# Performance work log

Hardware: AMD Instinct MI355X
Metric: run time of the kernel (lower is better)

The kernel has to match this reference:

```python
import math
import jax, jax.numpy as jnp
import numpy as np

B, C, H, W = 64, 1536, 16, 16
M_CLUSTERS, L_DIM, G_DIM, HID = 64, 128, 256, 512


def setup_inputs() -> dict:
    key = jax.random.key(0)
    ks = jax.random.split(key, 10)

    def w(k, out_d, in_d):
        return jax.random.normal(k, (out_d, in_d), jnp.float32) * (1.0 / np.sqrt(in_d))

    return {
        "x": jax.random.normal(ks[0], (B, C, H, W), jnp.float32),
        "t": jax.random.normal(ks[1], (B, C), jnp.float32),
        # token_features: Linear(C,512) -> ReLU -> Linear(512, token_dim)
        "Wt1": w(ks[2], HID, C), "bt1": jnp.zeros((HID,), jnp.float32),
        "Wt2": w(ks[3], G_DIM, HID), "bt2": jnp.zeros((G_DIM,), jnp.float32),
        # cluster_features: Conv1x1(C,512) -> ReLU -> Conv1x1(512, cluster_dim)
        "Wc1": w(ks[4], HID, C), "bc1": jnp.zeros((HID,), jnp.float32),
        "Wc2": w(ks[5], L_DIM, HID), "bc2": jnp.zeros((L_DIM,), jnp.float32),
        # score: Conv1x1(C,512) -> ReLU -> Conv1x1(512, num_clusters)
        "Ws1": w(ks[6], HID, C), "bs1": jnp.zeros((HID,), jnp.float32),
        "Ws2": w(ks[7], M_CLUSTERS, HID), "bs2": jnp.zeros((M_CLUSTERS,), jnp.float32),
        "dust_bin": jnp.float32(1.0),
    }


def _l2norm(a, axis):
    n = jnp.maximum(jnp.linalg.norm(a, axis=axis, keepdims=True), 1e-12)
    return a / n


def _conv1x1_mlp(xf, W1, b1, W2, b2):
    # xf: [B, C, N]; 1x1 convs are channel GEMMs
    h = jax.nn.relu(jnp.einsum('oc,bcn->bon', W1, xf) + b1[None, :, None])
    return jnp.einsum('oc,bcn->bon', W2, h) + b2[None, :, None]


def _matching_probs(S, dust_bin, num_iters=3):
    # Sinkhorn with dustbin row (log domain), reg = 1.0
    b, m, n = S.shape
    dust_row = jnp.broadcast_to(dust_bin.astype(S.dtype), (b, 1, n))
    Ms = jnp.concatenate([S, dust_row], axis=1)  # [B, m+1, n]
    norm = -math.log(n + m)
    log_a = jnp.full((m + 1,), norm, S.dtype).at[-1].add(math.log(n - m))
    log_b = jnp.full((n,), norm, S.dtype)
    u = jnp.zeros((b, m + 1), S.dtype)
    v = jnp.zeros((b, n), S.dtype)
    for _ in range(num_iters):
        u = log_a[None, :] - jax.scipy.special.logsumexp(Ms + v[:, None, :], axis=2)
        v = log_b[None, :] - jax.scipy.special.logsumexp(Ms + u[:, :, None], axis=1)
    return Ms + u[:, :, None] + v[:, None, :] - norm  # log_P - norm


def reference(x, t, Wt1, bt1, Wt2, bt2, Wc1, bc1, Wc2, bc2, Ws1, bs1, Ws2, bs2, dust_bin):
    b, c, h, w = x.shape
    n = h * w
    xf = x.reshape(b, c, n)
    f = _conv1x1_mlp(xf, Wc1, bc1, Wc2, bc2)      # [B, l, N]
    s = _conv1x1_mlp(xf, Ws1, bs1, Ws2, bs2)      # [B, m, N]
    tok = jax.nn.relu(t @ Wt1.T + bt1) @ Wt2.T + bt2  # [B, g]

    log_p = _matching_probs(s, dust_bin, num_iters=3)
    p = jnp.exp(log_p)[:, :-1, :]                 # drop dustbin row -> [B, m, N]

    # (f.unsqueeze(2) * p.unsqueeze(1)).sum(-1) is exactly a batched matmul
    vlad = jnp.einsum('bln,bmn->blm', f, p)       # [B, l, m]
    vlad = _l2norm(vlad, axis=1).reshape(b, -1)   # intra-norm over l, then flatten(1)

    out = jnp.concatenate([_l2norm(tok, axis=-1), vlad], axis=-1)
    return _l2norm(out, axis=-1)
```

## Files before the change

### kernel.cpp

```cpp
#include <hip/hip_runtime.h>
#include <math.h>

#define BNT 16384

using f32x4 = __attribute__((ext_vector_type(4))) float;
using s16x8 = __attribute__((ext_vector_type(8))) short;

__device__ __forceinline__ unsigned short f32_to_bf16_rne(float f) {
  unsigned int u = __float_as_uint(f);
  u += 0x7FFFu + ((u >> 16) & 1u);
  return (unsigned short)(u >> 16);
}
__device__ __forceinline__ unsigned pack_bf16x2(float a, float b) {
  return (unsigned)f32_to_bf16_rne(a) | ((unsigned)f32_to_bf16_rne(b) << 16);
}

__device__ __forceinline__ void gload_lds16(const ushort* g, ushort* lds) {
  __builtin_amdgcn_global_load_lds(
      (const __attribute__((address_space(1))) unsigned int*)g,
      (__attribute__((address_space(3))) unsigned int*)lds, 16, 0, 0);
}

__global__ __launch_bounds__(256) void prep_all2(
    const float* __restrict__ t, const float* __restrict__ Wt1,
    const float* __restrict__ Wt2, const float* __restrict__ Wc1,
    const float* __restrict__ Ws1, const float* __restrict__ bc1,
    const float* __restrict__ bs1, const float* __restrict__ Wc2,
    const float* __restrict__ Ws2, const float* __restrict__ bc2,
    const float* __restrict__ bs2, const float* __restrict__ x,
    ushort* __restrict__ Tb, ushort* __restrict__ Wt1b,
    ushort* __restrict__ Wt2b, ushort* __restrict__ Wc1b,
    ushort* __restrict__ Ws1b, float* __restrict__ b1,
    ushort* __restrict__ A2, float* __restrict__ b2,
    ushort* __restrict__ XT) {
  __shared__ ushort lds[16384];
  const int bid = blockIdx.x, tid = threadIdx.x;
  if (bid >= 2788) {
    const int tb = bid - 2788;
    const int b = tb / 24, cc = (tb % 24) * 64;
    const int tt = tid;
    const float* xb = x + b * 393216 + cc * 256;
#pragma unroll
    for (int i = 0; i < 16; ++i) {
      const int c0 = i * 4;
      const float v0 = xb[(c0 + 0) * 256 + tt];
      const float v1 = xb[(c0 + 1) * 256 + tt];
      const float v2 = xb[(c0 + 2) * 256 + tt];
      const float v3 = xb[(c0 + 3) * 256 + tt];
      uint2 o;
      o.x = pack_bf16x2(v0, v1);
      o.y = pack_bf16x2(v2, v3);
      const int g = c0 >> 3;
      const int waddr = tt * 128 + (((g ^ (tt & 7)) << 4) | ((c0 & 7) << 1));
      *(uint2*)((char*)lds + waddr) = o;
    }
    __syncthreads();
#pragma unroll
    for (int r = 0; r < 8; ++r) {
      const int j = r * 32 + (tt >> 3), q = tt & 7;
      const uint4 o =
          *(const uint4*)((const char*)lds + j * 128 + ((q ^ (j & 7)) << 4));
      *(uint4*)(XT + (size_t)(b * 256 + j) * 1536 + cc + q * 8) = o;
    }
    return;
  }
  const float* src = nullptr;
  ushort* dst = nullptr;
  int i = 0;
  if (bid < 96) {
    src = t; dst = Tb; i = bid * 256 + tid;
  } else if (bid < 864) {
    src = Wt1; dst = Wt1b; i = (bid - 96) * 256 + tid;
  } else if (bid < 992) {
    src = Wt2; dst = Wt2b; i = (bid - 864) * 256 + tid;
  } else if (bid < 1760) {
    src = Wc1; dst = Wc1b; i = (bid - 992) * 256 + tid;
  } else if (bid < 2528) {
    src = Ws1; dst = Ws1b; i = (bid - 1760) * 256 + tid;
  } else if (bid < 2532) {
    const int j = (bid - 2528) * 256 + tid;
    b1[j] = j < 512 ? bc1[j] : bs1[j - 512];
    return;
  } else {
    const int r = bid - 2532;
    const int c = tid * 4;
    float v[4] = {0.f, 0.f, 0.f, 0.f};
    if (r < 128) {
      if (c < 512) {
#pragma unroll
        for (int j = 0; j < 4; ++j) v[j] = Wc2[r * 512 + c + j];
      }
    } else if (r < 192) {
      if (c >= 512) {
#pragma unroll
        for (int j = 0; j < 4; ++j) v[j] = Ws2[(r - 128) * 512 + (c - 512) + j];
      }
    }
    uint2 o;
    o.x = pack_bf16x2(v[0], v[1]);
    o.y = pack_bf16x2(v[2], v[3]);
    *(uint2*)(A2 + r * 1024 + c) = o;
    if (tid == 0) b2[r] = r < 128 ? bc2[r] : (r < 192 ? bs2[r - 128] : 0.f);
    return;
  }
  const float4 v = ((const float4*)src)[i];
  uint2 o;
  o.x = pack_bf16x2(v.x, v.y);
  o.y = pack_bf16x2(v.z, v.w);
  ((uint2*)dst)[i] = o;
}

__global__ __launch_bounds__(256) void token1_mfma(
    const ushort* __restrict__ Tb, const ushort* __restrict__ Wt1b,
    float* __restrict__ Pt) {
  const int ct = blockIdx.x, kc = blockIdx.y;
  const int tid = threadIdx.x, l = tid & 63, wv = tid >> 6;
  const int lr = l & 15, ko = l >> 4;
  const int col = ct * 64 + wv * 16 + lr;
  f32x4 acc[4];
#pragma unroll
  for (int r = 0; r < 4; ++r) acc[r] = (f32x4){0.f, 0.f, 0.f, 0.f};
  const int k0 = kc * 384;
#pragma unroll 4
  for (int ks = 0; ks < 12; ++ks) {
    const int k = k0 + ks * 32 + ko * 8;
    const s16x8 bf = *(const s16x8*)(Wt1b + (size_t)col * 1536 + k);
#pragma unroll
    for (int rf = 0; rf < 4; ++rf) {
      const s16x8 af = *(const s16x8*)(Tb + (size_t)(rf * 16 + lr) * 1536 + k);
      acc[rf] =
          __builtin_amdgcn_mfma_f32_16x16x32_bf16(af, bf, acc[rf], 0, 0, 0);
    }
  }
#pragma unroll
  for (int rf = 0; rf < 4; ++rf)
#pragma unroll
    for (int j = 0; j < 4; ++j) {
      const int row = rf * 16 + ko * 4 + j;
      Pt[((kc * 64 + row) << 9) + col] = acc[rf][j];
    }
}

__global__ __launch_bounds__(256) void token1_reduce(
    const float* __restrict__ Pt, const float* __restrict__ bt1,
    ushort* __restrict__ Hb) {
  const int i = blockIdx.x * 256 + threadIdx.x;
  const int row = i >> 8, c2 = (i & 255) * 2;
  float v0 = bt1[c2], v1 = bt1[c2 + 1];
#pragma unroll
  for (int kc = 0; kc < 4; ++kc) {
    v0 += Pt[((kc * 64 + row) << 9) + c2];
    v1 += Pt[((kc * 64 + row) << 9) + c2 + 1];
  }
  v0 = fmaxf(v0, 0.f);
  v1 = fmaxf(v1, 0.f);
  ((unsigned*)Hb)[i] = pack_bf16x2(v0, v1);
}

__global__ __launch_bounds__(256) void token2_mfma(
    const ushort* __restrict__ Hb, const ushort* __restrict__ Wt2b,
    const float* __restrict__ bt2, float* __restrict__ TK) {
  const int ct = blockIdx.x;
  const int tid = threadIdx.x, l = tid & 63, wv = tid >> 6;
  const int lr = l & 15, ko = l >> 4;
  const int col = ct * 64 + wv * 16 + lr;
  f32x4 acc[4];
#pragma unroll
  for (int r = 0; r < 4; ++r) acc[r] = (f32x4){0.f, 0.f, 0.f, 0.f};
#pragma unroll 4
  for (int ks = 0; ks < 16; ++ks) {
    const int k = ks * 32 + ko * 8;
    const s16x8 bf = *(const s16x8*)(Wt2b + (size_t)col * 512 + k);
#pragma unroll
    for (int rf = 0; rf < 4; ++rf) {
      const s16x8 af = *(const s16x8*)(Hb + (size_t)(rf * 16 + lr) * 512 + k);
      acc[rf] =
          __builtin_amdgcn_mfma_f32_16x16x32_bf16(af, bf, acc[rf], 0, 0, 0);
    }
  }
  const float bb = bt2[col];
#pragma unroll
  for (int rf = 0; rf < 4; ++rf)
#pragma unroll
    for (int j = 0; j < 4; ++j)
      TK[(rf * 16 + ko * 4 + j) * 256 + col] = acc[rf][j] + bb;
}

__global__ __launch_bounds__(512) void gemm1_8ph(
    const ushort* __restrict__ A1, const ushort* __restrict__ Bt,
    const float* __restrict__ b1, ushort* __restrict__ HT) {
  __shared__ ushort lds[65536];
  const int tid = threadIdx.x, l = tid & 63, w = tid >> 6;
  const int bid = blockIdx.x;
  const int newid = (bid & 7) * 32 + (bid >> 3);
  const int m0 = (newid & 3) * 256, n0 = (newid >> 2) * 256;
  const int wr = w >> 2, wc = w & 3;
  const int lr = l & 15, kq = l >> 4;
  const int permK8 = (kq ^ ((lr >> 1) & 3)) * 8;
  const int aRow = wr * 128 + lr;
  const int bRow = wc * 64 + lr;

  f32x4 acc[8][4];
#pragma unroll
  for (int mi = 0; mi < 8; ++mi)
#pragma unroll
    for (int ni = 0; ni < 4; ++ni) acc[mi][ni] = (f32x4){0.f, 0.f, 0.f, 0.f};

  const int srow = tid >> 2, ssp = tid & 3;
  const int skq = ssp ^ ((srow >> 1) & 3);
  const ushort* sA0 = A1 + (size_t)(m0 + srow) * 1536 + skq * 8;
  const ushort* sA1 = A1 + (size_t)(m0 + srow + 128) * 1536 + skq * 8;
  const ushort* sB0 = Bt + (size_t)(n0 + srow) * 1536 + skq * 8;
  const ushort* sB1 = Bt + (size_t)(n0 + srow + 128) * 1536 + skq * 8;
  const int wofs = w * 512;

#define STG_A(tau, kh)                                              \
  do {                                                              \
    ushort* d = &lds[((((tau)&1) * 2 + (kh)) * 8192) + wofs];       \
    gload_lds16(sA0 + (tau)*64 + (kh)*32, d);                       \
    gload_lds16(sA1 + (tau)*64 + (kh)*32, d + 4096);                \
  } while (0)
#define STG_B(tau, kh)                                              \
  do {                                                              \
    ushort* d = &lds[32768 + ((((tau)&1) * 2 + (kh)) * 8192) + wofs]; \
    gload_lds16(sB0 + (tau)*64 + (kh)*32, d);                       \
    gload_lds16(sB1 + (tau)*64 + (kh)*32, d + 4096);                \
  } while (0)

  STG_A(0, 0);
  STG_B(0, 0);
  STG_A(0, 1);
  STG_B(0, 1);
  asm volatile("s_waitcnt vmcnt(0)" ::: "memory");
  __builtin_amdgcn_s_barrier();

  for (int sg = 0; sg < 24; ++sg) {
    const int rho = sg & 1;
    const int As0 = (rho * 2 + 0) * 8192, As1 = (rho * 2 + 1) * 8192;
    const int Bs0 = 32768 + As0, Bs1 = 32768 + As1;
    const bool st = (sg + 1) < 24;
    s16x8 af[4], bfv[4];

#pragma unroll
    for (int i = 0; i < 4; ++i)
      af[i] = *(const s16x8*)&lds[As0 + (aRow + i * 16) * 32 + permK8];
#pragma unroll
    for (int ni = 0; ni < 4; ++ni)
      bfv[ni] = *(const s16x8*)&lds[Bs0 + (bRow + ni * 16) * 32 + permK8];
    if (st) STG_A(sg + 1, 0);
    __builtin_amdgcn_s_barrier();
    __builtin_amdgcn_s_setprio(1);
#pragma unroll
    for (int i = 0; i < 4; ++i)
#pragma unroll
      for (int ni = 0; ni < 4; ++ni)
        acc[i][ni] = __builtin_amdgcn_mfma_f32_16x16x32_bf16(af[i], bfv[ni],
                                                             acc[i][ni], 0, 0, 0);
    __builtin_amdgcn_s_setprio(0);
    __builtin_amdgcn_s_barrier();

#pragma unroll
    for (int i = 0; i < 4; ++i)
      af[i] = *(const s16x8*)&lds[As0 + (aRow + 64 + i * 16) * 32 + permK8];
    if (st) STG_B(sg + 1, 0);
    if (sg < 23)
      asm volatile("s_waitcnt vmcnt(4)" ::: "memory");
    else
      asm volatile("s_waitcnt vmcnt(0)" ::: "memory");
    __builtin_amdgcn_s_barrier();
    __builtin_amdgcn_s_setprio(1);
#pragma unroll
    for (int i = 0; i < 4; ++i)
#pragma unroll
      for (int ni = 0; ni < 4; ++ni)
        acc[4 + i][ni] = __builtin_amdgcn_mfma_f32_16x16x32_bf16(
            af[i], bfv[ni], acc[4 + i][ni], 0, 0, 0);
    __builtin_amdgcn_s_setprio(0);
    __builtin_amdgcn_s_barrier();

#pragma unroll
    for (int i = 0; i < 4; ++i)
      af[i] = *(const s16x8*)&lds[As1 + (aRow + i * 16) * 32 + permK8];
#pragma unroll
    for (int ni = 0; ni < 4; ++ni)
      bfv[ni] = *(const s16x8*)&lds[Bs1 + (bRow + ni * 16) * 32 + permK8];
    if (st) STG_A(sg + 1, 1);
    __builtin_amdgcn_s_barrier();
    __builtin_amdgcn_s_setprio(1);
#pragma unroll
    for (int i = 0; i < 4; ++i)
#pragma unroll
      for (int ni = 0; ni < 4; ++ni)
        acc[i][ni] = __builtin_amdgcn_mfma_f32_16x16x32_bf16(af[i], bfv[ni],
                                                             acc[i][ni], 0, 0, 0);
    __builtin_amdgcn_s_setprio(0);
    __builtin_amdgcn_s_barrier();

#pragma unroll
    for (int i = 0; i < 4; ++i)
      af[i] = *(const s16x8*)&lds[As1 + (aRow + 64 + i * 16) * 32 + permK8];
    if (st) STG_B(sg + 1, 1);
    asm volatile("s_waitcnt vmcnt(4)" ::: "memory");
    __builtin_amdgcn_s_barrier();
    __builtin_amdgcn_s_setprio(1);
#pragma unroll
    for (int i = 0; i < 4; ++i)
#pragma unroll
      for (int ni = 0; ni < 4; ++ni)
        acc[4 + i][ni] = __builtin_amdgcn_mfma_f32_16x16x32_bf16(
            af[i], bfv[ni], acc[4 + i][ni], 0, 0, 0);
    __builtin_amdgcn_s_setprio(0);
    __builtin_amdgcn_s_barrier();
  }
#undef STG_A
#undef STG_B

#pragma unroll
  for (int mi = 0; mi < 8; ++mi) {
    const int rbase = m0 + wr * 128 + mi * 16 + kq * 4;
    float b4[4];
#pragma unroll
    for (int j = 0; j < 4; ++j) b4[j] = b1[rbase + j];
#pragma unroll
    for (int ni = 0; ni < 4; ++ni) {
      const int col = n0 + wc * 64 + ni * 16 + lr;
      const float v0 = fmaxf(acc[mi][ni][0] + b4[0], 0.f);
      const float v1 = fmaxf(acc[mi][ni][1] + b4[1], 0.f);
      const float v2 = fmaxf(acc[mi][ni][2] + b4[2], 0.f);
      const float v3 = fmaxf(acc[mi][ni][3] + b4[3], 0.f);
      uint2 o;
      o.x = pack_bf16x2(v0, v1);
      o.y = pack_bf16x2(v2, v3);
      *(uint2*)(HT + (size_t)col * 1024 + rbase) = o;
    }
  }
}

__global__ __launch_bounds__(256) void gemm2_mfma64(
    const ushort* __restrict__ A2, const ushort* __restrict__ HT,
    const float* __restrict__ b2, float* __restrict__ C2,
    ushort* __restrict__ Fb) {
  constexpr int K = 1024;
  __shared__ ushort As[2 * 6144];
  __shared__ ushort Bs[2 * 8192];
  const int tid = threadIdx.x;
  const int l = tid & 63, w = tid >> 6;
  const int bid = blockIdx.x;
  const int newid = (bid & 7) * 32 + (bid >> 3);
  const int m0 = (newid & 1) * 96, n0 = (newid >> 1) * 128;
  const int wr = w >> 1, wc = w & 1;
  const int lr = l & 15, kq = l >> 4;

  f32x4 acc[3][4];
#pragma unroll
  for (int mi = 0; mi < 3; ++mi)
#pragma unroll
    for (int ni = 0; ni < 4; ++ni) acc[mi][ni] = (f32x4){0.f, 0.f, 0.f, 0.f};

  const ushort* srcA[3];
#pragma unroll
  for (int j = 0; j < 3; ++j) {
    const int g = tid + j * 256;
    const int q = g & 3, r2 = g >> 2;
    const int sub = r2 / 96, r = r2 - sub * 96;
    srcA[j] = A2 + (size_t)(m0 + r) * K + (sub * 4 + q) * 8;
  }
  const ushort* srcB[4];
#pragma unroll
  for (int j = 0; j < 4; ++j) {
    const int g = tid + j * 256;
    const int q = g & 3, r2 = g >> 2;
    const int r = r2 & 127, sub = r2 >> 7;
    srcB[j] = HT + (size_t)(n0 + r) * K + (sub * 4 + q) * 8;
  }
  const int wofs = w * 512;

#define STAGE2(k0v, buf)                                               \
  do {                                                                 \
    gload_lds16(srcA[0] + (k0v), As + (buf)*6144 + 0 * 2048 + wofs);   \
    gload_lds16(srcA[1] + (k0v), As + (buf)*6144 + 1 * 2048 + wofs);   \
    gload_lds16(srcA[2] + (k0v), As + (buf)*6144 + 2 * 2048 + wofs);   \
    gload_lds16(srcB[0] + (k0v), Bs + (buf)*8192 + 0 * 2048 + wofs);   \
    gload_lds16(srcB[1] + (k0v), Bs + (buf)*8192 + 1 * 2048 + wofs);   \
    gload_lds16(srcB[2] + (k0v), Bs + (buf)*8192 + 2 * 2048 + wofs);   \
    gload_lds16(srcB[3] + (k0v), Bs + (buf)*8192 + 3 * 2048 + wofs);   \
  } while (0)

  STAGE2(0, 0);
  __syncthreads();

  int cur = 0;
  for (int k0 = 0; k0 < K; k0 += 64) {
    const int nxt = cur ^ 1;
    if (k0 + 64 < K) STAGE2(k0 + 64, nxt);
    const ushort* Ab = As + cur * 6144;
    const ushort* Bb = Bs + cur * 8192;
#pragma unroll
    for (int s = 0; s < 2; ++s) {
      s16x8 af[3], bfr[4];
#pragma unroll
      for (int mi = 0; mi < 3; ++mi)
        af[mi] = *(const s16x8*)(Ab + (s * 96 + wr * 48 + mi * 16 + lr) * 32 +
                                 kq * 8);
#pragma unroll
      for (int ni = 0; ni < 4; ++ni)
        bfr[ni] = *(const s16x8*)(Bb + (s * 128 + wc * 64 + ni * 16 + lr) * 32 +
                                  kq * 8);
#pragma unroll
      for (int mi = 0; mi < 3; ++mi)
#pragma unroll
        for (int ni = 0; ni < 4; ++ni)
          acc[mi][ni] = __builtin_amdgcn_mfma_f32_16x16x32_bf16(
              af[mi], bfr[ni], acc[mi][ni], 0, 0, 0);
    }
    __syncthreads();
    cur = nxt;
  }
#undef STAGE2

#pragma unroll
  for (int mi = 0; mi < 3; ++mi) {
    const int rbase = m0 + wr * 48 + mi * 16 + kq * 4;
    float b4[4];
#pragma unroll
    for (int j = 0; j < 4; ++j) b4[j] = b2[rbase + j];
    if (rbase < 128) {
#pragma unroll
      for (int ni = 0; ni < 4; ++ni) {
        const int col = n0 + wc * 64 + ni * 16 + lr;
#pragma unroll
        for (int j = 0; j < 4; ++j)
          Fb[(size_t)(rbase + j) * BNT + col] =
              f32_to_bf16_rne(acc[mi][ni][j] + b4[j]);
      }
    } else {
#pragma unroll
      for (int ni = 0; ni < 4; ++ni) {
        const int col = n0 + wc * 64 + ni * 16 + lr;
        float* cr = C2 + (size_t)rbase * BNT + col;
#pragma unroll
        for (int j = 0; j < 4; ++j) cr[(size_t)j * BNT] = acc[mi][ni][j] + b4[j];
      }
    }
  }
}

__global__ __launch_bounds__(256) void post_kernel(
    const float* __restrict__ S, const float* __restrict__ dustp,
    const ushort* __restrict__ Fb, const float* __restrict__ TK,
    float* __restrict__ out) {
  __shared__ char smem[100672];
  float(*E)[256] = (float(*)[256])smem;
  float* U = (float*)(smem + 66560);
  float* V = (float*)(smem + 66880);
  ushort* Pl = (ushort*)(smem + 67904);
  float* VLs = (float*)smem;
  float* sred = (float*)(smem + 32768);
  float* ssm = (float*)(smem + 32784);
  float* invm_s = (float*)(smem + 33808);
  float* totals = (float*)(smem + 34064);

  const int b = blockIdx.x, tid = threadIdx.x;
  const int lane = tid & 63, wave = tid >> 6;

  for (int idx = tid; idx < 16384; idx += 256) {
    const int m = idx >> 8, n = idx & 255;
    E[m][n] = expf(S[m * BNT + b * 256 + n]);
  }
  E[64][tid] = expf(dustp[0]);
  V[tid] = 1.f;
  const float Ai = 1.f / 320.f;
  const float Adust = 192.f / 320.f;
  const float Bn = 1.f / 320.f;
  __syncthreads();
  for (int it = 0; it < 3; ++it) {
    for (int i = wave; i < 65; i += 4) {
      float s = E[i][lane] * V[lane];
      s = fmaf(E[i][lane + 64], V[lane + 64], s);
      s = fmaf(E[i][lane + 128], V[lane + 128], s);
      s = fmaf(E[i][lane + 192], V[lane + 192], s);
#pragma unroll
      for (int off = 32; off; off >>= 1) s += __shfl_xor(s, off);
      if (lane == 0) U[i] = (i == 64 ? Adust : Ai) / s;
    }
    __syncthreads();
    {
      const int n = tid;
      float s = 0.f;
#pragma unroll 13
      for (int i = 0; i < 65; ++i) s = fmaf(E[i][n], U[i], s);
      V[n] = Bn / s;
    }
    __syncthreads();
  }
#pragma unroll
  for (int j = 0; j < 8; ++j) {
    const int gg = tid + j * 256;
    const int row = gg >> 5, gr = gg & 31;
    const float um = U[row];
    const int n0g = gr * 8;
    float p[8];
#pragma unroll
    for (int e = 0; e < 8; ++e)
      p[e] = E[row][n0g + e] * um * V[n0g + e] * 320.f;
    uint4 o;
    o.x = pack_bf16x2(p[0], p[1]);
    o.y = pack_bf16x2(p[2], p[3]);
    o.z = pack_bf16x2(p[4], p[5]);
    o.w = pack_bf16x2(p[6], p[7]);
    *(uint4*)(Pl + row * 256 + ((gr ^ (row & 7)) << 3)) = o;
  }
  __syncthreads();
  const int l = lane, w = wave;
  const int lr = l & 15, ko = l >> 4;
  f32x4 acc[2][4];
#pragma unroll
  for (int li = 0; li < 2; ++li)
#pragma unroll
    for (int ni = 0; ni < 4; ++ni) acc[li][ni] = (f32x4){0.f, 0.f, 0.f, 0.f};
  const ushort* Fbase = Fb + b * 256;
#pragma unroll
  for (int ks = 0; ks < 8; ++ks) {
    s16x8 bfr[4];
#pragma unroll
    for (int ni = 0; ni < 4; ++ni) {
      const int row = ni * 16 + lr;
      const int gk = ks * 4 + ko;
      bfr[ni] = *(const s16x8*)(Pl + row * 256 + ((gk ^ (row & 7)) << 3));
    }
    const int k = ks * 32 + ko * 8;
#pragma unroll
    for (int li = 0; li < 2; ++li) {
      const s16x8 af =
          *(const s16x8*)(Fbase + (size_t)(w * 32 + li * 16 + lr) * BNT + k);
#pragma unroll
      for (int ni = 0; ni < 4; ++ni)
        acc[li][ni] = __builtin_amdgcn_mfma_f32_16x16x32_bf16(
            af, bfr[ni], acc[li][ni], 0, 0, 0);
    }
  }
#pragma unroll
  for (int li = 0; li < 2; ++li)
#pragma unroll
    for (int ni = 0; ni < 4; ++ni)
#pragma unroll
      for (int j = 0; j < 4; ++j) {
        const int ll = w * 32 + li * 16 + ko * 4 + j;
        const int m = ni * 16 + lr;
        VLs[ll * 64 + m] = acc[li][ni][j];
      }
  __syncthreads();
  float accv = 0.f;
  for (int k = 0; k < 32; ++k) {
    const float xv = VLs[tid + 256 * k];
    accv = fmaf(xv, xv, accv);
  }
  ssm[wave * 64 + lane] = accv;
  const float tv = TK[b * 256 + tid];
  float ss = tv * tv;
#pragma unroll
  for (int off = 32; off; off >>= 1) ss += __shfl_down(ss, off);
  if (lane == 0) sred[wave] = ss;
  __syncthreads();
  const float sstok = sred[0] + sred[1] + sred[2] + sred[3];
  const float invtok = 1.f / fmaxf(sqrtf(sstok), 1e-12f);
  float tpart = 0.f;
  if (wave == 0) {
    const float s4 =
        ssm[tid] + ssm[64 + tid] + ssm[128 + tid] + ssm[192 + tid];
    const float inv = 1.f / fmaxf(sqrtf(s4), 1e-12f);
    invm_s[tid] = inv;
    tpart = s4 * inv * inv;
#pragma unroll
    for (int off = 32; off; off >>= 1) tpart += __shfl_down(tpart, off);
    if (lane == 0) totals[0] = tpart;
  }
  __syncthreads();
  const float total = totals[0] + sstok * invtok * invtok;
  const float invT = 1.f / fmaxf(sqrtf(total), 1e-12f);
  float* ob = &out[b * 8448];
  ob[tid] = tv * invtok * invT;
  for (int k = 0; k < 32; ++k) {
    const int idx = tid + 256 * k;
    ob[256 + idx] = VLs[idx] * invm_s[idx & 63] * invT;
  }
}

__global__ __launch_bounds__(256) void finalize_kernel(
    const float* __restrict__ TK, const float* __restrict__ VL,
    float* __restrict__ out) {
  const int b = blockIdx.x, tid = threadIdx.x;
  const int lane = tid & 63, wave = tid >> 6;
  __shared__ float sred[4];
  __shared__ float ssm_part[4][64];
  __shared__ float invm_s[64];
  __shared__ float totals[1];
  const float* vl = &VL[b * 8192];
  float accv = 0.f;
  for (int k = 0; k < 32; ++k) {
    const float xv = vl[tid + 256 * k];
    accv = fmaf(xv, xv, accv);
  }
  ssm_part[wave][lane] = accv;
  const float tv = TK[b * 256 + tid];
  float ss = tv * tv;
#pragma unroll
  for (int off = 32; off; off >>= 1) ss += __shfl_down(ss, off);
  if (lane == 0) sred[wave] = ss;
  __syncthreads();
  const float sstok = sred[0] + sred[1] + sred[2] + sred[3];
  const float invtok = 1.f / fmaxf(sqrtf(sstok), 1e-12f);
  float tpart = 0.f;
  if (wave == 0) {
    const float s4 = ssm_part[0][tid] + ssm_part[1][tid] + ssm_part[2][tid] +
                     ssm_part[3][tid];
    const float inv = 1.f / fmaxf(sqrtf(s4), 1e-12f);
    invm_s[tid] = inv;
    tpart = s4 * inv * inv;
#pragma unroll
    for (int off = 32; off; off >>= 1) tpart += __shfl_down(tpart, off);
    if (lane == 0) totals[0] = tpart;
  }
  __syncthreads();
  const float total = totals[0] + sstok * invtok * invtok;
  const float invT = 1.f / fmaxf(sqrtf(total), 1e-12f);
  float* ob = &out[b * 8448];
  ob[tid] = tv * invtok * invT;
  for (int k = 0; k < 32; ++k) {
    const int idx = tid + 256 * k;
    ob[256 + idx] = vl[idx] * invm_s[idx & 63] * invT;
  }
}

template <bool RELU>
__global__ __launch_bounds__(256) void gemm_tt(
    const float* __restrict__ A, const float* __restrict__ Bw,
    const float* __restrict__ bias, float* __restrict__ C, int K, int Nn) {
  __shared__ float As[16][68];
  __shared__ float Bs[16][68];
  const int tid = threadIdx.x;
  const int tx = tid & 15, ty = tid >> 4;
  const int n0 = blockIdx.x * 64;
  const int lrow = tid >> 2, lkq = (tid & 3) << 2;
  float acc[4][4];
#pragma unroll
  for (int r = 0; r < 4; ++r)
#pragma unroll
    for (int c = 0; c < 4; ++c) acc[r][c] = 0.f;
  for (int k0 = 0; k0 < K; k0 += 16) {
    const float4 av = *(const float4*)&A[lrow * K + k0 + lkq];
    const float4 bv = *(const float4*)&Bw[(n0 + lrow) * K + k0 + lkq];
    As[lkq + 0][lrow] = av.x;
    As[lkq + 1][lrow] = av.y;
    As[lkq + 2][lrow] = av.z;
    As[lkq + 3][lrow] = av.w;
    Bs[lkq + 0][lrow] = bv.x;
    Bs[lkq + 1][lrow] = bv.y;
    Bs[lkq + 2][lrow] = bv.z;
    Bs[lkq + 3][lrow] = bv.w;
    __syncthreads();
#pragma unroll
    for (int kk = 0; kk < 16; ++kk) {
      const float4 a4 = *(const float4*)&As[kk][ty << 2];
      const float4 b4 = *(const float4*)&Bs[kk][tx << 2];
      acc[0][0] = fmaf(a4.x, b4.x, acc[0][0]);
      acc[0][1] = fmaf(a4.x, b4.y, acc[0][1]);
      acc[0][2] = fmaf(a4.x, b4.z, acc[0][2]);
      acc[0][3] = fmaf(a4.x, b4.w, acc[0][3]);
      acc[1][0] = fmaf(a4.y, b4.x, acc[1][0]);
      acc[1][1] = fmaf(a4.y, b4.y, acc[1][1]);
      acc[1][2] = fmaf(a4.y, b4.z, acc[1][2]);
      acc[1][3] = fmaf(a4.y, b4.w, acc[1][3]);
      acc[2][0] = fmaf(a4.z, b4.x, acc[2][0]);
      acc[2][1] = fmaf(a4.z, b4.y, acc[2][1]);
      acc[2][2] = fmaf(a4.z, b4.z, acc[2][2]);
      acc[2][3] = fmaf(a4.z, b4.w, acc[2][3]);
      acc[3][0] = fmaf(a4.w, b4.x, acc[3][0]);
      acc[3][1] = fmaf(a4.w, b4.y, acc[3][1]);
      acc[3][2] = fmaf(a4.w, b4.z, acc[3][2]);
      acc[3][3] = fmaf(a4.w, b4.w, acc[3][3]);
    }
    __syncthreads();
  }
#pragma unroll
  for (int r = 0; r < 4; ++r) {
    const int row = (ty << 2) + r;
    float4 o;
    o.x = acc[r][0] + bias[n0 + (tx << 2) + 0];
    o.y = acc[r][1] + bias[n0 + (tx << 2) + 1];
    o.z = acc[r][2] + bias[n0 + (tx << 2) + 2];
    o.w = acc[r][3] + bias[n0 + (tx << 2) + 3];
    if (RELU) {
      o.x = fmaxf(o.x, 0.f);
      o.y = fmaxf(o.y, 0.f);
      o.z = fmaxf(o.z, 0.f);
      o.w = fmaxf(o.w, 0.f);
    }
    *(float4*)&C[row * Nn + n0 + (tx << 2)] = o;
  }
}

template <bool XVIEW, bool RELU>
__global__ __launch_bounds__(256) void gemm_tile(
    const float* __restrict__ A, const float* __restrict__ Bsrc,
    const float* __restrict__ bias, float* __restrict__ Cout, int K) {
  __shared__ float As[16][68];
  __shared__ float Bsh[16][68];
  const int tid = threadIdx.x;
  const int tx = tid & 15, ty = tid >> 4;
  const int rowBase = blockIdx.y * 64;
  const int colBase = blockIdx.x * 64;
  const int bb = colBase >> 8, n0 = colBase & 255;
  const int boff = XVIEW ? (bb * 393216 + n0) : colBase;
  const int la_row = tid >> 2, la_kq = (tid & 3) << 2;
  const int lb_k = tid >> 4, lb_c = (tid & 15) << 2;
  float acc[4][4];
#pragma unroll
  for (int r = 0; r < 4; ++r)
#pragma unroll
    for (int c = 0; c < 4; ++c) acc[r][c] = 0.f;
  for (int k0 = 0; k0 < K; k0 += 16) {
    const float4 av = *(const float4*)&A[(rowBase + la_row) * K + k0 + la_kq];
    float4 bv;
    if (XVIEW)
      bv = *(const float4*)&Bsrc[boff + (k0 + lb_k) * 256 + lb_c];
    else
      bv = *(const float4*)&Bsrc[(k0 + lb_k) * BNT + boff + lb_c];
    As[la_kq + 0][la_row] = av.x;
    As[la_kq + 1][la_row] = av.y;
    As[la_kq + 2][la_row] = av.z;
    As[la_kq + 3][la_row] = av.w;
    *(float4*)&Bsh[lb_k][lb_c] = bv;
    __syncthreads();
#pragma unroll
    for (int kk = 0; kk < 16; ++kk) {
      const float4 a4 = *(const float4*)&As[kk][ty << 2];
      const float4 b4 = *(const float4*)&Bsh[kk][tx << 2];
      acc[0][0] = fmaf(a4.x, b4.x, acc[0][0]);
      acc[0][1] = fmaf(a4.x, b4.y, acc[0][1]);
      acc[0][2] = fmaf(a4.x, b4.z, acc[0][2]);
      acc[0][3] = fmaf(a4.x, b4.w, acc[0][3]);
      acc[1][0] = fmaf(a4.y, b4.x, acc[1][0]);
      acc[1][1] = fmaf(a4.y, b4.y, acc[1][1]);
      acc[1][2] = fmaf(a4.y, b4.z, acc[1][2]);
      acc[1][3] = fmaf(a4.y, b4.w, acc[1][3]);
      acc[2][0] = fmaf(a4.z, b4.x, acc[2][0]);
      acc[2][1] = fmaf(a4.z, b4.y, acc[2][1]);
      acc[2][2] = fmaf(a4.z, b4.z, acc[2][2]);
      acc[2][3] = fmaf(a4.z, b4.w, acc[2][3]);
      acc[3][0] = fmaf(a4.w, b4.x, acc[3][0]);
      acc[3][1] = fmaf(a4.w, b4.y, acc[3][1]);
      acc[3][2] = fmaf(a4.w, b4.z, acc[3][2]);
      acc[3][3] = fmaf(a4.w, b4.w, acc[3][3]);
    }
    __syncthreads();
  }
#pragma unroll
  for (int r = 0; r < 4; ++r) {
    const int row = rowBase + (ty << 2) + r;
    const float bsv = bias[row];
    float4 o;
    o.x = acc[r][0] + bsv;
    o.y = acc[r][1] + bsv;
    o.z = acc[r][2] + bsv;
    o.w = acc[r][3] + bsv;
    if (RELU) {
      o.x = fmaxf(o.x, 0.f);
      o.y = fmaxf(o.y, 0.f);
      o.z = fmaxf(o.z, 0.f);
      o.w = fmaxf(o.w, 0.f);
    }
    *(float4*)&Cout[row * BNT + colBase + (tx << 2)] = o;
  }
}

__global__ __launch_bounds__(256) void sinkhorn_kernel(
    const float* __restrict__ S, const float* __restrict__ dustp,
    float* __restrict__ P) {
  const int b = blockIdx.x, tid = threadIdx.x;
  const int lane = tid & 63, wave = tid >> 6;
  __shared__ float Ms[65][256];
  __shared__ float u[65];
  __shared__ float v[256];
  const float dust = dustp[0];
  for (int idx = tid; idx < 16384; idx += 256) {
    const int m = idx >> 8, n = idx & 255;
    Ms[m][n] = S[m * BNT + b * 256 + n];
  }
  Ms[64][tid] = dust;
  v[tid] = 0.f;
  if (tid < 65) u[tid] = 0.f;
  const float norm = -logf(320.f);
  const float la_dust = norm + logf(192.f);
  __syncthreads();
  for (int it = 0; it < 3; ++it) {
    for (int i = wave; i < 65; i += 4) {
      const float x0 = Ms[i][lane] + v[lane];
      const float x1 = Ms[i][lane + 64] + v[lane + 64];
      const float x2 = Ms[i][lane + 128] + v[lane + 128];
      const float x3 = Ms[i][lane + 192] + v[lane + 192];
      float mm = fmaxf(fmaxf(x0, x1), fmaxf(x2, x3));
#pragma unroll
      for (int off = 32; off; off >>= 1) mm = fmaxf(mm, __shfl_xor(mm, off));
      float s = expf(x0 - mm) + expf(x1 - mm) + expf(x2 - mm) + expf(x3 - mm);
#pragma unroll
      for (int off = 32; off; off >>= 1) s += __shfl_xor(s, off);
      if (lane == 0) u[i] = (i == 64 ? la_dust : norm) - (logf(s) + mm);
    }
    __syncthreads();
    {
      const int n = tid;
      float mm = -1e30f;
      for (int i = 0; i < 65; ++i) mm = fmaxf(mm, Ms[i][n] + u[i]);
      float s = 0.f;
      for (int i = 0; i < 65; ++i) s += expf(Ms[i][n] + u[i] - mm);
      v[n] = norm - (logf(s) + mm);
    }
    __syncthreads();
  }
  for (int idx = tid; idx < 16384; idx += 256) {
    const int m = idx >> 8, n = idx & 255;
    P[b * 16384 + idx] = expf(Ms[m][n] + u[m] + v[n] - norm);
  }
}

__device__ __forceinline__ int ps_idx(int m, int n) {
  return m * 256 + ((((n >> 2) ^ (m & 7)) << 2) | (n & 3));
}
__global__ __launch_bounds__(256) void vlad_kernel(const float* __restrict__ F,
                                                   const float* __restrict__ P,
                                                   float* __restrict__ VL) {
  const int b = blockIdx.x, half = blockIdx.y;
  const int tid = threadIdx.x;
  const int m = tid & 63, lg = tid >> 6;
  __shared__ float ps[64 * 256];
  for (int idx = tid; idx < 16384; idx += 256) {
    const int mm = idx >> 8, n = idx & 255;
    ps[ps_idx(mm, n)] = P[b * 16384 + idx];
  }
  __syncthreads();
  float acc[16];
#pragma unroll
  for (int i = 0; i < 16; ++i) acc[i] = 0.f;
  for (int i = 0; i < 16; ++i) {
    const int ll = half * 64 + lg + 4 * i;
    const float* frow = &F[(size_t)ll * BNT + b * 256];
    float a = 0.f;
#pragma unroll 8
    for (int nq = 0; nq < 64; ++nq) {
      const float4 f4 = *(const float4*)&frow[nq << 2];
      const float4 p4 = *(const float4*)&ps[m * 256 + ((nq ^ (m & 7)) << 2)];
      a = fmaf(f4.x, p4.x, a);
      a = fmaf(f4.y, p4.y, a);
      a = fmaf(f4.z, p4.z, a);
      a = fmaf(f4.w, p4.w, a);
    }
    acc[i] = a;
  }
#pragma unroll
  for (int i = 0; i < 16; ++i) {
    const int ll = half * 64 + lg + 4 * i;
    VL[b * 8192 + ll * 64 + m] = acc[i];
  }
}

extern "C" void kernel_launch(void* const* d_in, const int* in_sizes, int n_in,
                              void* d_out, int out_size, void* d_ws,
                              size_t ws_size, hipStream_t stream) {
  const float* x = (const float*)d_in[0];
  const float* t = (const float*)d_in[1];
  const float* Wt1 = (const float*)d_in[2];
  const float* bt1 = (const float*)d_in[3];
  const float* Wt2 = (const float*)d_in[4];
  const float* bt2 = (const float*)d_in[5];
  const float* Wc1 = (const float*)d_in[6];
  const float* bc1 = (const float*)d_in[7];
  const float* Wc2 = (const float*)d_in[8];
  const float* bc2 = (const float*)d_in[9];
  const float* Ws1 = (const float*)d_in[10];
  const float* bs1 = (const float*)d_in[11];
  const float* Ws2 = (const float*)d_in[12];
  const float* bs2 = (const float*)d_in[13];
  const float* dust = (const float*)d_in[14];
  float* out = (float*)d_out;

  if (ws_size >= 97714176ull) {
    char* base = (char*)d_ws;
    ushort* XT = (ushort*)base;
    ushort* Tb = (ushort*)(base + 50331648);
    ushort* Wt1b = (ushort*)(base + 50528256);
    ushort* Wt2b = (ushort*)(base + 52101120);
    float* Pt = (float*)(base + 52363264);
    ushort* Hb = (ushort*)(base + 52887552);
    ushort* Fb = (ushort*)(base + 8388608);
    ushort* HT = (ushort*)(base + 50331648);
    float* C2 = (float*)(base + 83886080);
    ushort* A1 = (ushort*)(base + 83886080);
    ushort* Wc1b = A1;
    ushort* Ws1b = (ushort*)(base + 85458944);
    ushort* A2 = (ushort*)(base + 96468992);
    float* b2 = (float*)(base + 96993280);
    float* TK = (float*)(base + 96994304);
    float* b1 = (float*)(base + 97059840);
    float* Sb = C2 + (size_t)128 * BNT;

    prep_all2<<<4324, 256, 0, stream>>>(t, Wt1, Wt2, Wc1, Ws1, bc1, bs1, Wc2,
                                        Ws2, bc2, bs2, x, Tb, Wt1b, Wt2b, Wc1b,
                                        Ws1b, b1, A2, b2, XT);
    token1_mfma<<<dim3(8, 4), 256, 0, stream>>>(Tb, Wt1b, Pt);
    token1_reduce<<<64, 256, 0, stream>>>(Pt, bt1, Hb);
    token2_mfma<<<4, 256, 0, stream>>>(Hb, Wt2b, bt2, TK);
    gemm1_8ph<<<256, 512, 0, stream>>>(A1, XT, b1, HT);
    gemm2_mfma64<<<256, 256, 0, stream>>>(A2, HT, b2, C2, Fb);
    post_kernel<<<64, 256, 0, stream>>>(Sb, dust, Fb, TK, out);
  } else {
    float* ws = (float*)d_ws;
    float* H = ws;
    float* F = H + 512 * BNT;
    float* Sb = F + 128 * BNT;
    float* P = Sb + 64 * BNT;
    float* VL = P + 64 * BNT;
    float* TK = VL + 64 * 8192;
    float* Hh = P;

    gemm_tt<true><<<dim3(8, 1), 256, 0, stream>>>(t, Wt1, bt1, Hh, 1536, 512);
    gemm_tt<false><<<dim3(4, 1), 256, 0, stream>>>(Hh, Wt2, bt2, TK, 512, 256);
    gemm_tile<true, true><<<dim3(256, 8), 256, 0, stream>>>(Wc1, x, bc1, H, 1536);
    gemm_tile<false, false><<<dim3(256, 2), 256, 0, stream>>>(Wc2, H, bc2, F, 512);
    gemm_tile<true, true><<<dim3(256, 8), 256, 0, stream>>>(Ws1, x, bs1, H, 1536);
    gemm_tile<false, false><<<dim3(256, 1), 256, 0, stream>>>(Ws2, H, bs2, Sb, 512);
    sinkhorn_kernel<<<64, 256, 0, stream>>>(Sb, dust, P);
    vlad_kernel<<<dim3(64, 2), 256, 0, stream>>>(F, P, VL);
    finalize_kernel<<<64, 256, 0, stream>>>(TK, VL, out);
  }
}
```

Measured before the change: 152.1 us.

## Fuse token split-K reduce into full-K kernel; widen post kernel to 512 threads

The token first-layer GEMM now runs the full K loop in one kernel and applies bias, ReLU and the bf16 store directly, which removes the split-K partial buffer and the separate reduce launch. This cuts the parallelism of that GEMM to 8 blocks, each with a four-times longer serial loop. The post kernel goes from 256 to 512 threads so the exp, Sinkhorn row sums and VLAD MFMA work are split across 8 waves. Several phases are guarded to the first 256 threads, leaving half the block idle during them.

```diff
diff --git a/kernel.cpp b/kernel.cpp
--- a/kernel.cpp
+++ b/kernel.cpp
@@ -110,20 +110,19 @@
   ((uint2*)dst)[i] = o;
 }
 
-__global__ __launch_bounds__(256) void token1_mfma(
+__global__ __launch_bounds__(256) void token1_fullk(
     const ushort* __restrict__ Tb, const ushort* __restrict__ Wt1b,
-    float* __restrict__ Pt) {
-  const int ct = blockIdx.x, kc = blockIdx.y;
+    const float* __restrict__ bt1, ushort* __restrict__ Hb) {
+  const int ct = blockIdx.x;
   const int tid = threadIdx.x, l = tid & 63, wv = tid >> 6;
   const int lr = l & 15, ko = l >> 4;
   const int col = ct * 64 + wv * 16 + lr;
   f32x4 acc[4];
 #pragma unroll
   for (int r = 0; r < 4; ++r) acc[r] = (f32x4){0.f, 0.f, 0.f, 0.f};
-  const int k0 = kc * 384;
 #pragma unroll 4
-  for (int ks = 0; ks < 12; ++ks) {
-    const int k = k0 + ks * 32 + ko * 8;
+  for (int ks = 0; ks < 48; ++ks) {
+    const int k = ks * 32 + ko * 8;
     const s16x8 bf = *(const s16x8*)(Wt1b + (size_t)col * 1536 + k);
 #pragma unroll
     for (int rf = 0; rf < 4; ++rf) {
@@ -132,29 +131,14 @@
           __builtin_amdgcn_mfma_f32_16x16x32_bf16(af, bf, acc[rf], 0, 0, 0);
     }
   }
+  const float bb = bt1[col];
 #pragma unroll
   for (int rf = 0; rf < 4; ++rf)
 #pragma unroll
     for (int j = 0; j < 4; ++j) {
       const int row = rf * 16 + ko * 4 + j;
-      Pt[((kc * 64 + row) << 9) + col] = acc[rf][j];
-    }
-}
-
-__global__ __launch_bounds__(256) void token1_reduce(
-    const float* __restrict__ Pt, const float* __restrict__ bt1,
-    ushort* __restrict__ Hb) {
-  const int i = blockIdx.x * 256 + threadIdx.x;
-  const int row = i >> 8, c2 = (i & 255) * 2;
-  float v0 = bt1[c2], v1 = bt1[c2 + 1];
-#pragma unroll
-  for (int kc = 0; kc < 4; ++kc) {
-    v0 += Pt[((kc * 64 + row) << 9) + c2];
-    v1 += Pt[((kc * 64 + row) << 9) + c2 + 1];
-  }
-  v0 = fmaxf(v0, 0.f);
-  v1 = fmaxf(v1, 0.f);
-  ((unsigned*)Hb)[i] = pack_bf16x2(v0, v1);
+      Hb[row * 512 + col] = f32_to_bf16_rne(fmaxf(acc[rf][j] + bb, 0.f));
+    }
 }
 
 __global__ __launch_bounds__(256) void token2_mfma(
@@ -445,7 +429,7 @@
   }
 }
 
-__global__ __launch_bounds__(256) void post_kernel(
+__global__ __launch_bounds__(512) void post_kernel(
     const float* __restrict__ S, const float* __restrict__ dustp,
     const ushort* __restrict__ Fb, const float* __restrict__ TK,
     float* __restrict__ out) {
@@ -463,18 +447,20 @@
   const int b = blockIdx.x, tid = threadIdx.x;
   const int lane = tid & 63, wave = tid >> 6;
 
-  for (int idx = tid; idx < 16384; idx += 256) {
+  for (int idx = tid; idx < 16384; idx += 512) {
     const int m = idx >> 8, n = idx & 255;
     E[m][n] = expf(S[m * BNT + b * 256 + n]);
   }
-  E[64][tid] = expf(dustp[0]);
-  V[tid] = 1.f;
+  if (tid < 256) {
+    E[64][tid] = expf(dustp[0]);
+    V[tid] = 1.f;
+  }
   const float Ai = 1.f / 320.f;
   const float Adust = 192.f / 320.f;
   const float Bn = 1.f / 320.f;
   __syncthreads();
   for (int it = 0; it < 3; ++it) {
-    for (int i = wave; i < 65; i += 4) {
+    for (int i = wave; i < 65; i += 8) {
       float s = E[i][lane] * V[lane];
       s = fmaf(E[i][lane + 64], V[lane + 64], s);
       s = fmaf(E[i][lane + 128], V[lane + 128], s);
@@ -484,7 +470,7 @@
       if (lane == 0) U[i] = (i == 64 ? Adust : Ai) / s;
     }
     __syncthreads();
-    {
+    if (tid < 256) {
       const int n = tid;
       float s = 0.f;
 #pragma unroll 13
@@ -494,8 +480,8 @@
     __syncthreads();
   }
 #pragma unroll
-  for (int j = 0; j < 8; ++j) {
-    const int gg = tid + j * 256;
+  for (int j = 0; j < 4; ++j) {
+    const int gg = tid + j * 512;
     const int row = gg >> 5, gr = gg & 31;
     const float um = U[row];
     const int n0g = gr * 8;
@@ -511,13 +497,10 @@
     *(uint4*)(Pl + row * 256 + ((gr ^ (row & 7)) << 3)) = o;
   }
   __syncthreads();
-  const int l = lane, w = wave;
-  const int lr = l & 15, ko = l >> 4;
-  f32x4 acc[2][4];
-#pragma unroll
-  for (int li = 0; li < 2; ++li)
-#pragma unroll
-    for (int ni = 0; ni < 4; ++ni) acc[li][ni] = (f32x4){0.f, 0.f, 0.f, 0.f};
+  const int lr = lane & 15, ko = lane >> 4;
+  f32x4 acc[4];
+#pragma unroll
+  for (int ni = 0; ni < 4; ++ni) acc[ni] = (f32x4){0.f, 0.f, 0.f, 0.f};
   const ushort* Fbase = Fb + b * 256;
 #pragma unroll
   for (int ks = 0; ks < 8; ++ks) {
@@ -529,60 +512,59 @@
       bfr[ni] = *(const s16x8*)(Pl + row * 256 + ((gk ^ (row & 7)) << 3));
     }
     const int k = ks * 32 + ko * 8;
-#pragma unroll
-    for (int li = 0; li < 2; ++li) {
-      const s16x8 af =
-          *(const s16x8*)(Fbase + (size_t)(w * 32 + li * 16 + lr) * BNT + k);
-#pragma unroll
-      for (int ni = 0; ni < 4; ++ni)
-        acc[li][ni] = __builtin_amdgcn_mfma_f32_16x16x32_bf16(
-            af, bfr[ni], acc[li][ni], 0, 0, 0);
-    }
-  }
-#pragma unroll
-  for (int li = 0; li < 2; ++li)
+    const s16x8 af =
+        *(const s16x8*)(Fbase + (size_t)(wave * 16 + lr) * BNT + k);
 #pragma unroll
     for (int ni = 0; ni < 4; ++ni)
-#pragma unroll
-      for (int j = 0; j < 4; ++j) {
-        const int ll = w * 32 + li * 16 + ko * 4 + j;
-        const int m = ni * 16 + lr;
-        VLs[ll * 64 + m] = acc[li][ni][j];
-      }
+      acc[ni] = __builtin_amdgcn_mfma_f32_16x16x32_bf16(af, bfr[ni], acc[ni],
+                                                        0, 0, 0);
+  }
+#pragma unroll
+  for (int ni = 0; ni < 4; ++ni)
+#pragma unroll
+    for (int j = 0; j < 4; ++j) {
+      const int ll = wave * 16 + ko * 4 + j;
+      const int m = ni * 16 + lr;
+      VLs[ll * 64 + m] = acc[ni][j];
+    }
   __syncthreads();
-  float accv = 0.f;
-  for (int k = 0; k < 32; ++k) {
-    const float xv = VLs[tid + 256 * k];
-    accv = fmaf(xv, xv, accv);
-  }
-  ssm[wave * 64 + lane] = accv;
-  const float tv = TK[b * 256 + tid];
-  float ss = tv * tv;
-#pragma unroll
-  for (int off = 32; off; off >>= 1) ss += __shfl_down(ss, off);
-  if (lane == 0) sred[wave] = ss;
+  if (tid < 256) {
+    float accv = 0.f;
+    for (int k = 0; k < 32; ++k) {
+      const float xv = VLs[tid + 256 * k];
+      accv = fmaf(xv, xv, accv);
+    }
+    ssm[wave * 64 + lane] = accv;
+    const float tv = TK[b * 256 + tid];
+    float ss = tv * tv;
+#pragma unroll
+    for (int off = 32; off; off >>= 1) ss += __shfl_down(ss, off);
+    if (lane == 0) sred[wave] = ss;
+  }
   __syncthreads();
   const float sstok = sred[0] + sred[1] + sred[2] + sred[3];
   const float invtok = 1.f / fmaxf(sqrtf(sstok), 1e-12f);
-  float tpart = 0.f;
-  if (wave == 0) {
+  if (tid < 64) {
     const float s4 =
         ssm[tid] + ssm[64 + tid] + ssm[128 + tid] + ssm[192 + tid];
     const float inv = 1.f / fmaxf(sqrtf(s4), 1e-12f);
     invm_s[tid] = inv;
-    tpart = s4 * inv * inv;
+    float tpart = s4 * inv * inv;
 #pragma unroll
     for (int off = 32; off; off >>= 1) tpart += __shfl_down(tpart, off);
-    if (lane == 0) totals[0] = tpart;
+    if (tid == 0) totals[0] = tpart;
   }
   __syncthreads();
-  const float total = totals[0] + sstok * invtok * invtok;
-  const float invT = 1.f / fmaxf(sqrtf(total), 1e-12f);
-  float* ob = &out[b * 8448];
-  ob[tid] = tv * invtok * invT;
-  for (int k = 0; k < 32; ++k) {
-    const int idx = tid + 256 * k;
-    ob[256 + idx] = VLs[idx] * invm_s[idx & 63] * invT;
+  if (tid < 256) {
+    const float total = totals[0] + sstok * invtok * invtok;
+    const float invT = 1.f / fmaxf(sqrtf(total), 1e-12f);
+    const float tv = TK[b * 256 + tid];
+    float* ob = &out[b * 8448];
+    ob[tid] = tv * invtok * invT;
+    for (int k = 0; k < 32; ++k) {
+      const int idx = tid + 256 * k;
+      ob[256 + idx] = VLs[idx] * invm_s[idx & 63] * invT;
+    }
   }
 }
 
@@ -890,7 +872,6 @@
     ushort* Tb = (ushort*)(base + 50331648);
     ushort* Wt1b = (ushort*)(base + 50528256);
     ushort* Wt2b = (ushort*)(base + 52101120);
-    float* Pt = (float*)(base + 52363264);
     ushort* Hb = (ushort*)(base + 52887552);
     ushort* Fb = (ushort*)(base + 8388608);
     ushort* HT = (ushort*)(base + 50331648);
@@ -907,12 +888,11 @@
     prep_all2<<<4324, 256, 0, stream>>>(t, Wt1, Wt2, Wc1, Ws1, bc1, bs1, Wc2,
                                         Ws2, bc2, bs2, x, Tb, Wt1b, Wt2b, Wc1b,
                                         Ws1b, b1, A2, b2, XT);
-    token1_mfma<<<dim3(8, 4), 256, 0, stream>>>(Tb, Wt1b, Pt);
-    token1_reduce<<<64, 256, 0, stream>>>(Pt, bt1, Hb);
+    token1_fullk<<<8, 256, 0, stream>>>(Tb, Wt1b, bt1, Hb);
     token2_mfma<<<4, 256, 0, stream>>>(Hb, Wt2b, bt2, TK);
     gemm1_8ph<<<256, 512, 0, stream>>>(A1, XT, b1, HT);
     gemm2_mfma64<<<256, 256, 0, stream>>>(A2, HT, b2, C2, Fb);
-    post_kernel<<<64, 256, 0, stream>>>(Sb, dust, Fb, TK, out);
+    post_kernel<<<64, 512, 0, stream>>>(Sb, dust, Fb, TK, out);
   } else {
     float* ws = (float*)d_ws;
     float* H = ws;
```

New measurement: 160.8 us. +5.7%, slower.
